# Performance work log

Measured on AMD Instinct MI355X. Metric: run time of the kernel, lower is better.

The kernel has to match this reference:

```python
import jax, jax.numpy as jnp
import numpy as np

B, S, D = 4, 2048, 1024

def setup_inputs() -> dict:
    key = jax.random.key(0)
    kv, kk, kq, kw = jax.random.split(key, 4)
    scale = 1.0 / np.sqrt(D)
    v = jax.random.normal(kv, (B, S, D), dtype=jnp.float32)
    k = jax.random.normal(kk, (B, S, D), dtype=jnp.float32)
    q = jax.random.normal(kq, (B, S, D), dtype=jnp.float32)
    wi = jax.random.normal(kw, (D, D), dtype=jnp.float32) * scale
    mask = jnp.tril(jnp.ones((S, S), dtype=bool))[None, :, :]  # causal [1,S,S]
    return {"v": v, "k": k, "q": q, "wi": wi, "mask": mask}

def reference(v, k, q, wi, mask):
    # project q, k, v with the shared weight wi
    q = q @ wi
    k = k @ wi
    v = v @ wi
    # scaled dot-product scores [B,S,S]
    scores = jnp.einsum('bqd,bkd->bqk', q, k) / jnp.sqrt(jnp.asarray(q.shape[-1], q.dtype))
    scores = jnp.where(mask, scores, jnp.asarray(-1e10, scores.dtype))
    attn = jax.nn.softmax(scores, axis=-1)
    # residual: q + attn @ v
    return q + jnp.einsum('bqk,bkd->bqd', attn, v)
```

## Files before the change

kernel.cpp:

```cpp
#include <hip/hip_runtime.h>
#include <hip/hip_bf16.h>

typedef __hip_bfloat16 bf16;
typedef short bf16x8 __attribute__((ext_vector_type(8)));
typedef float f32x4 __attribute__((ext_vector_type(4)));

#define HT 16384

__device__ __forceinline__ void gload16(const void* g, void* l) {
    __builtin_amdgcn_global_load_lds(
        (const __attribute__((address_space(1))) void*)g,
        (__attribute__((address_space(3))) void*)l, 16, 0, 0);
}

__device__ __forceinline__ void stage_half(char* lds, const bf16* src, int ld,
                                           int rowbase, int k0, int slotIdx,
                                           int tid)
{
    char* dst = lds + (size_t)slotIdx * HT + tid * 16;
    const int sub = tid >> 3;
    const int cb  = ((tid & 7) ^ (sub & 7)) << 4;
    #pragma unroll
    for (int p = 0; p < 2; ++p) {
        const int row = p * 64 + sub;
        const char* g = (const char*)(src + (size_t)(rowbase + row) * ld + k0) + cb;
        gload16(g, dst + p * 8192);
    }
}

__device__ __forceinline__ bf16x8 ldsfrag(const char* lds, int slotIdx,
                                          int row, int ks, int cb0)
{
    return *(const bf16x8*)(lds + (size_t)slotIdx * HT
                            + row * 128 + (cb0 ^ (ks << 6)));
}

__device__ __forceinline__ float bf2f(short s) {
    union { float f; unsigned u; } c;
    c.u = ((unsigned)(unsigned short)s) << 16;
    return c.f;
}

__launch_bounds__(512, 2)
__global__ void proj_bn128(const bf16* __restrict__ A, const bf16* __restrict__ B,
                           bf16* __restrict__ C)
{
    extern __shared__ char lds[];
    const int orig = blockIdx.y * 8 + blockIdx.x;
    const int wk = (orig & 7) * 96 + (orig >> 3);
    const int bi = wk >> 3, bj = wk & 7;
    const int brow = bi * 256, bcol = bj * 128;

    const int tid  = threadIdx.x;
    const int lane = tid & 63;
    const int w    = tid >> 6;
    const int wm   = w >> 1, wn = w & 1;
    const int fr   = lane & 15, fq = lane >> 4;
    const int cb0  = ((fr & 7) ^ fq) << 4;
    const int slotA = wm >> 1;
    const int rA    = (wm & 1) * 64;
    const int rB    = wn * 64;
    const int NT    = 16;

    f32x4 acc[4][4] = {};
    bf16x8 af[4][2], bv[4][2];

    stage_half(lds, B, 1024, bcol,       0, 2, tid);
    stage_half(lds, A, 1024, brow,       0, 0, tid);
    stage_half(lds, A, 1024, brow + 128, 0, 1, tid);
    stage_half(lds, B, 1024, bcol,      64, 5, tid);
    asm volatile("s_waitcnt vmcnt(2)" ::: "memory");
    __builtin_amdgcn_s_barrier();

#define QUAD2(m0, n0)                                                         \
    _Pragma("unroll") for (int dm = 0; dm < 2; ++dm)                          \
    _Pragma("unroll") for (int dn = 0; dn < 2; ++dn)                          \
    _Pragma("unroll") for (int ks = 0; ks < 2; ++ks)                          \
        acc[(m0)+dm][(n0)+dn] = __builtin_amdgcn_mfma_f32_16x16x32_bf16(      \
            af[(m0)+dm][ks], bv[(n0)+dn][ks], acc[(m0)+dm][(n0)+dn], 0, 0, 0);

    for (int t = 0; t < NT; ++t) {
        const int buf = t & 1, nbuf = buf ^ 1;
        const int k1 = min(t + 1, NT - 1) << 6;
        const int k2 = min(t + 2, NT - 1) << 6;

        #pragma unroll
        for (int m = 0; m < 2; ++m)
            #pragma unroll
            for (int ks = 0; ks < 2; ++ks)
                af[m][ks] = ldsfrag(lds, buf * 3 + slotA, rA + m * 16 + fr, ks, cb0);
        #pragma unroll
        for (int n = 0; n < 2; ++n)
            #pragma unroll
            for (int ks = 0; ks < 2; ++ks)
                bv[n][ks] = ldsfrag(lds, buf * 3 + 2, rB + n * 16 + fr, ks, cb0);
        stage_half(lds, A, 1024, brow, k1, nbuf * 3 + 0, tid);
        __builtin_amdgcn_s_barrier();
        __builtin_amdgcn_s_setprio(1);
        QUAD2(0, 0)
        __builtin_amdgcn_s_setprio(0);
        __builtin_amdgcn_s_barrier();

        #pragma unroll
        for (int n = 2; n < 4; ++n)
            #pragma unroll
            for (int ks = 0; ks < 2; ++ks)
                bv[n][ks] = ldsfrag(lds, buf * 3 + 2, rB + n * 16 + fr, ks, cb0);
        stage_half(lds, A, 1024, brow + 128, k1, nbuf * 3 + 1, tid);
        __builtin_amdgcn_s_barrier();
        __builtin_amdgcn_s_setprio(1);
        QUAD2(0, 2)
        __builtin_amdgcn_s_setprio(0);
        __builtin_amdgcn_s_barrier();

        #pragma unroll
        for (int m = 2; m < 4; ++m)
            #pragma unroll
            for (int ks = 0; ks < 2; ++ks)
                af[m][ks] = ldsfrag(lds, buf * 3 + slotA, rA + m * 16 + fr, ks, cb0);
        stage_half(lds, B, 1024, bcol, k2, buf * 3 + 2, tid);
        __builtin_amdgcn_s_barrier();
        __builtin_amdgcn_s_setprio(1);
        QUAD2(2, 2)
        __builtin_amdgcn_s_setprio(0);
        __builtin_amdgcn_s_barrier();

        __builtin_amdgcn_s_setprio(1);
        QUAD2(2, 0)
        __builtin_amdgcn_s_setprio(0);
        asm volatile("s_waitcnt vmcnt(2)" ::: "memory");
        __builtin_amdgcn_s_barrier();
    }
#undef QUAD2

    #pragma unroll
    for (int mf = 0; mf < 4; ++mf) {
        const int r0 = brow + wm * 64 + mf * 16 + fq * 4;
        #pragma unroll
        for (int nf = 0; nf < 4; ++nf) {
            const int c = bcol + wn * 64 + nf * 16 + fr;
            #pragma unroll
            for (int j = 0; j < 4; ++j)
                C[(size_t)(r0 + j) * 1024 + c] = __float2bfloat16(acc[mf][nf][j]);
        }
    }
}

template<int MODE>
__device__ __forceinline__ void tile128(char* lds, const bf16* A, const bf16* B,
                                        bf16* Cb, float* Cf, const bf16* Res,
                                        int lda, int ldb, int ldcb,
                                        int brow, int bcol, int NT, float scale,
                                        int tid, int wm, int wn, int fr, int fq,
                                        int cb0)
{
    f32x4 acc[4][2] = {};
    bf16x8 af[4][2], bv[2][2];

    stage_half(lds, A, lda, brow, 0,  0, tid);
    stage_half(lds, B, ldb, bcol, 0,  3, tid);
    stage_half(lds, A, lda, brow, 64, 1, tid);
    stage_half(lds, B, ldb, bcol, 64, 4, tid);
    asm volatile("s_waitcnt vmcnt(4)" ::: "memory");
    __builtin_amdgcn_s_barrier();

    for (int t = 0; t < NT; ++t) {
        const int aslot = t % 3, bslot = 3 + (t & 1);
        const int k2 = min(t + 2, NT - 1) << 6;

        #pragma unroll
        for (int m = 0; m < 2; ++m)
            #pragma unroll
            for (int ks = 0; ks < 2; ++ks)
                af[m][ks] = ldsfrag(lds, aslot, wm * 64 + m * 16 + fr, ks, cb0);
        #pragma unroll
        for (int n = 0; n < 2; ++n)
            #pragma unroll
            for (int ks = 0; ks < 2; ++ks)
                bv[n][ks] = ldsfrag(lds, bslot, wn * 32 + n * 16 + fr, ks, cb0);
        stage_half(lds, A, lda, brow, k2, (t + 2) % 3, tid);
        __builtin_amdgcn_s_barrier();
        __builtin_amdgcn_s_setprio(1);
        #pragma unroll
        for (int m = 0; m < 2; ++m)
            #pragma unroll
            for (int n = 0; n < 2; ++n)
                #pragma unroll
                for (int ks = 0; ks < 2; ++ks)
                    acc[m][n] = __builtin_amdgcn_mfma_f32_16x16x32_bf16(
                        af[m][ks], bv[n][ks], acc[m][n], 0, 0, 0);
        __builtin_amdgcn_s_setprio(0);
        __builtin_amdgcn_s_barrier();

        #pragma unroll
        for (int m = 2; m < 4; ++m)
            #pragma unroll
            for (int ks = 0; ks < 2; ++ks)
                af[m][ks] = ldsfrag(lds, aslot, wm * 64 + m * 16 + fr, ks, cb0);
        stage_half(lds, B, ldb, bcol, k2, bslot, tid);
        __builtin_amdgcn_s_barrier();
        __builtin_amdgcn_s_setprio(1);
        #pragma unroll
        for (int m = 2; m < 4; ++m)
            #pragma unroll
            for (int n = 0; n < 2; ++n)
                #pragma unroll
                for (int ks = 0; ks < 2; ++ks)
                    acc[m][n] = __builtin_amdgcn_mfma_f32_16x16x32_bf16(
                        af[m][ks], bv[n][ks], acc[m][n], 0, 0, 0);
        __builtin_amdgcn_s_setprio(0);
        asm volatile("s_waitcnt vmcnt(4)" ::: "memory");
        __builtin_amdgcn_s_barrier();
    }

    #pragma unroll
    for (int mf = 0; mf < 4; ++mf) {
        const int r0 = brow + wm * 64 + mf * 16 + fq * 4;
        #pragma unroll
        for (int nf = 0; nf < 2; ++nf) {
            const int c = bcol + wn * 32 + nf * 16 + fr;
            #pragma unroll
            for (int j = 0; j < 4; ++j) {
                if (MODE == 1)
                    Cb[(size_t)(r0 + j) * ldcb + c] =
                        __float2bfloat16(acc[mf][nf][j] * scale);
                else
                    Cf[(size_t)(r0 + j) * ldcb + c] = acc[mf][nf][j] +
                        __bfloat162float(Res[(size_t)(r0 + j) * ldcb + c]);
            }
        }
    }
}

__launch_bounds__(512, 4)
__global__ void scores128(const bf16* __restrict__ qp, const bf16* __restrict__ kp,
                          bf16* __restrict__ P)
{
    extern __shared__ char lds[];
    const int j = blockIdx.x;
    int bi = (int)((__fsqrt_rn(8.0f * j + 1.0f) - 1.0f) * 0.5f);
    while ((bi + 1) * (bi + 2) / 2 <= j) ++bi;
    while (bi * (bi + 1) / 2 > j) --bi;
    const int bj = j - bi * (bi + 1) / 2;
    const int bz = blockIdx.z;

    const int tid  = threadIdx.x;
    const int lane = tid & 63;
    const int w    = tid >> 6;
    const int wm   = w >> 2, wn = w & 3;
    const int fr   = lane & 15, fq = lane >> 4;
    const int cb0  = ((fr & 7) ^ fq) << 4;

    tile128<1>(lds,
               qp + (size_t)bz * 2048 * 1024,
               kp + (size_t)bz * 2048 * 1024,
               P + (size_t)bz * 2048 * 2048, nullptr, nullptr,
               1024, 1024, 2048,
               bi * 128, bj * 128, 16, 0.03125f,
               tid, wm, wn, fr, fq, cb0);
}

__launch_bounds__(512, 4)
__global__ void pv128(const bf16* __restrict__ P, const bf16* __restrict__ V,
                      const bf16* __restrict__ R, float* __restrict__ C)
{
    extern __shared__ char lds[];
    const int pid = blockIdx.x, bj = blockIdx.y, bz = blockIdx.z;
    const bf16* Pb = P + (size_t)bz * 2048 * 2048;
    const bf16* Vb = V + (size_t)bz * 1024 * 2048;
    const bf16* Rb = R + (size_t)bz * 2048 * 1024;
    float* Cb = C + (size_t)bz * 2048 * 1024;

    const int tid  = threadIdx.x;
    const int lane = tid & 63;
    const int w    = tid >> 6;
    const int wm   = w >> 2, wn = w & 3;
    const int fr   = lane & 15, fq = lane >> 4;
    const int cb0  = ((fr & 7) ^ fq) << 4;
    const int bcol = bj * 128;

    tile128<2>(lds, Pb, Vb, nullptr, Cb, Rb, 2048, 2048, 1024,
               pid * 128, bcol, 2 * (pid + 1), 1.0f,
               tid, wm, wn, fr, fq, cb0);
    asm volatile("s_waitcnt vmcnt(0) lgkmcnt(0)" ::: "memory");
    __builtin_amdgcn_s_barrier();
    const int bi2 = 15 - pid;
    tile128<2>(lds, Pb, Vb, nullptr, Cb, Rb, 2048, 2048, 1024,
               bi2 * 128, bcol, 2 * (bi2 + 1), 1.0f,
               tid, wm, wn, fr, fq, cb0);
}

__global__ void convert_qkv(const float* __restrict__ q, const float* __restrict__ k,
                            const float* __restrict__ v, bf16* __restrict__ Xb)
{
    const int N8 = 8192 * 1024 / 8;
    const int total = 3 * N8;
    for (int i = blockIdx.x * 256 + threadIdx.x; i < total; i += gridDim.x * 256) {
        const int t = i / N8, j = i - t * N8;
        const float4* s = (t == 0) ? (const float4*)q
                        : (t == 1) ? (const float4*)k : (const float4*)v;
        float4 a = s[2 * j], bq = s[2 * j + 1];
        float vals[8] = {a.x, a.y, a.z, a.w, bq.x, bq.y, bq.z, bq.w};
        union { short h[8]; bf16x8 v8; } o;
        #pragma unroll
        for (int e = 0; e < 8; ++e) {
            bf16 hh = __float2bfloat16(vals[e]);
            o.h[e] = *(short*)&hh;
        }
        ((bf16x8*)Xb)[i] = o.v8;
    }
}

__global__ void transpose_wi(const float* __restrict__ wi, bf16* __restrict__ Wt)
{
    __shared__ float t[32][33];
    const int n0 = blockIdx.x * 32, k0 = blockIdx.y * 32;
    const int lx = threadIdx.x & 31, ly = threadIdx.x >> 5;
    for (int i = ly; i < 32; i += 8)
        t[i][lx] = wi[(size_t)(k0 + i) * 1024 + n0 + lx];
    __syncthreads();
    for (int i = ly; i < 32; i += 8)
        Wt[(size_t)(n0 + i) * 1024 + k0 + lx] = __float2bfloat16(t[lx][i]);
}

__global__ void transpose_vp(const bf16* __restrict__ vp, bf16* __restrict__ vpT)
{
    __shared__ bf16 t[32][33];
    const int b = blockIdx.z;
    const int d0 = blockIdx.x * 32, s0 = blockIdx.y * 32;
    const bf16* src = vp + (size_t)b * 2048 * 1024;
    bf16* dst = vpT + (size_t)b * 1024 * 2048;
    const int lx = threadIdx.x & 31, ly = threadIdx.x >> 5;
    for (int i = ly; i < 32; i += 8)
        t[i][lx] = src[(size_t)(s0 + i) * 1024 + d0 + lx];
    __syncthreads();
    for (int i = ly; i < 32; i += 8)
        dst[(size_t)(d0 + i) * 2048 + s0 + lx] = t[lx][i];
}

__launch_bounds__(256)
__global__ void softmax_rows(bf16* __restrict__ P)
{
    const int wid = threadIdx.x >> 6, lane = threadIdx.x & 63;
    const int r = blockIdx.x * 4 + wid, b = blockIdx.y;
    bf16* row = P + ((size_t)b * 2048 + r) * 2048;
    const int nv  = r + 1;
    const int rup = (r & ~255) + 256;

    float vals[4][8];
    float m = -1e30f;
    #pragma unroll
    for (int c = 0; c < 4; ++c) {
        const int k0 = c * 512 + lane * 8;
        if (k0 < rup) {
            bf16x8 x = *(const bf16x8*)(row + k0);
            #pragma unroll
            for (int j = 0; j < 8; ++j) {
                float f = (k0 + j < nv) ? bf2f(x[j]) : -1e30f;
                vals[c][j] = f;
                m = fmaxf(m, f);
            }
        } else {
            #pragma unroll
            for (int j = 0; j < 8; ++j) vals[c][j] = -1e30f;
        }
    }
    #pragma unroll
    for (int o = 32; o; o >>= 1) m = fmaxf(m, __shfl_xor(m, o));

    float sum = 0.f;
    #pragma unroll
    for (int c = 0; c < 4; ++c)
        #pragma unroll
        for (int j = 0; j < 8; ++j) {
            float e = __expf(vals[c][j] - m);
            vals[c][j] = e;
            sum += e;
        }
    #pragma unroll
    for (int o = 32; o; o >>= 1) sum += __shfl_xor(sum, o);
    const float inv = 1.0f / sum;

    #pragma unroll
    for (int c = 0; c < 4; ++c) {
        const int k0 = c * 512 + lane * 8;
        if (k0 < rup) {
            union { short h[8]; bf16x8 v8; } o;
            #pragma unroll
            for (int j = 0; j < 8; ++j) {
                bf16 hh = __float2bfloat16(vals[c][j] * inv);
                o.h[j] = *(short*)&hh;
            }
            *(bf16x8*)(row + k0) = o.v8;
        }
    }
}

extern "C" void kernel_launch(void* const* d_in, const int* in_sizes, int n_in,
                              void* d_out, int out_size, void* d_ws, size_t ws_size,
                              hipStream_t stream)
{
    const float* v  = (const float*)d_in[0];
    const float* k  = (const float*)d_in[1];
    const float* q  = (const float*)d_in[2];
    const float* wi = (const float*)d_in[3];
    float* out = (float*)d_out;

    char* ws = (char*)d_ws;
    const size_t WT_OFF   = 0;
    const size_t PROJ_OFF = WT_OFF + (2u << 20);
    const size_t VPT_OFF  = PROJ_OFF + (size_t)24576 * 1024 * 2;
    const size_t XB_OFF   = VPT_OFF + (size_t)4 * 1024 * 2048 * 2;

    bf16* Wt   = (bf16*)(ws + WT_OFF);
    bf16* proj = (bf16*)(ws + PROJ_OFF);
    bf16* vpT  = (bf16*)(ws + VPT_OFF);
    bf16* Xb   = (bf16*)(ws + XB_OFF);
    bf16* P    = Xb;

    bf16* qp_b = proj;
    bf16* kp_b = proj + (size_t)8192 * 1024;
    bf16* vp_b = proj + (size_t)16384 * 1024;

    (void)hipFuncSetAttribute((const void*)proj_bn128,
            hipFuncAttributeMaxDynamicSharedMemorySize, 98304);
    (void)hipFuncSetAttribute((const void*)scores128,
            hipFuncAttributeMaxDynamicSharedMemorySize, 81920);
    (void)hipFuncSetAttribute((const void*)pv128,
            hipFuncAttributeMaxDynamicSharedMemorySize, 81920);

    transpose_wi<<<dim3(32, 32), 256, 0, stream>>>(wi, Wt);
    convert_qkv<<<2048, 256, 0, stream>>>(q, k, v, Xb);

    proj_bn128<<<dim3(8, 96), 512, 98304, stream>>>(Xb, Wt, proj);

    transpose_vp<<<dim3(32, 64, 4), 256, 0, stream>>>(vp_b, vpT);

    scores128<<<dim3(136, 1, 4), 512, 81920, stream>>>(qp_b, kp_b, P);

    softmax_rows<<<dim3(512, 4), 256, 0, stream>>>(P);

    pv128<<<dim3(8, 8, 4), 512, 81920, stream>>>(P, vpT, qp_b, out);
}
```

Measured before the change: 183.7 us.

## Fuse V transpose into projection epilogue and split-K warps in attention tiles

The projection kernel now writes the V projection directly in transposed layout from its epilogue, so the separate transpose_vp kernel and its extra global round trip go away. The shared tile128 routine is restructured so that pairs of waves split the K dimension, each computing a full 64x64 subtile, with the partial sums reduced through LDS before the epilogue. The pv128 grid is reordered so batch varies fastest within blockIdx.x, and softmax_rows now rounds its read bound to 128 columns instead of 256. The transposed V stores are strided short4 writes that may coalesce poorly, and the split-K reduction adds an LDS pass plus more accumulator registers per wave.

```diff
diff --git a/kernel.cpp b/kernel.cpp
--- a/kernel.cpp
+++ b/kernel.cpp
@@ -43,12 +43,12 @@
 
 __launch_bounds__(512, 2)
 __global__ void proj_bn128(const bf16* __restrict__ A, const bf16* __restrict__ B,
-                           bf16* __restrict__ C)
+                           bf16* __restrict__ C, bf16* __restrict__ vpT)
 {
     extern __shared__ char lds[];
     const int orig = blockIdx.y * 8 + blockIdx.x;
-    const int wk = (orig & 7) * 96 + (orig >> 3);
-    const int bi = wk >> 3, bj = wk & 7;
+    const int wk2 = (orig & 7) * 96 + (orig >> 3);
+    const int bi = wk2 >> 3, bj = wk2 & 7;
     const int brow = bi * 256, bcol = bj * 128;
 
     const int tid  = threadIdx.x;
@@ -133,15 +133,36 @@
     }
 #undef QUAD2
 
-    #pragma unroll
-    for (int mf = 0; mf < 4; ++mf) {
-        const int r0 = brow + wm * 64 + mf * 16 + fq * 4;
-        #pragma unroll
-        for (int nf = 0; nf < 4; ++nf) {
-            const int c = bcol + wn * 64 + nf * 16 + fr;
-            #pragma unroll
-            for (int j = 0; j < 4; ++j)
-                C[(size_t)(r0 + j) * 1024 + c] = __float2bfloat16(acc[mf][nf][j]);
+    if (brow < 16384) {
+        #pragma unroll
+        for (int mf = 0; mf < 4; ++mf) {
+            const int r0 = brow + wm * 64 + mf * 16 + fq * 4;
+            #pragma unroll
+            for (int nf = 0; nf < 4; ++nf) {
+                const int c = bcol + wn * 64 + nf * 16 + fr;
+                #pragma unroll
+                for (int j = 0; j < 4; ++j)
+                    C[(size_t)(r0 + j) * 1024 + c] = __float2bfloat16(acc[mf][nf][j]);
+            }
+        }
+    } else {
+        const int bb = (brow - 16384) >> 11;
+        bf16* vt = vpT + (size_t)bb * 1024 * 2048;
+        #pragma unroll
+        for (int mf = 0; mf < 4; ++mf) {
+            const int r0 = brow + wm * 64 + mf * 16 + fq * 4;
+            const int s0 = (r0 - 16384) & 2047;
+            #pragma unroll
+            for (int nf = 0; nf < 4; ++nf) {
+                const int c = bcol + wn * 64 + nf * 16 + fr;
+                union { short h[4]; short4 v4; } o;
+                #pragma unroll
+                for (int j = 0; j < 4; ++j) {
+                    bf16 hh = __float2bfloat16(acc[mf][nf][j]);
+                    o.h[j] = *(short*)&hh;
+                }
+                *(short4*)(vt + (size_t)c * 2048 + s0) = o.v4;
+            }
         }
     }
 }
@@ -151,11 +172,18 @@
                                         bf16* Cb, float* Cf, const bf16* Res,
                                         int lda, int ldb, int ldcb,
                                         int brow, int bcol, int NT, float scale,
-                                        int tid, int wm, int wn, int fr, int fq,
-                                        int cb0)
-{
-    f32x4 acc[4][2] = {};
-    bf16x8 af[4][2], bv[2][2];
+                                        int tid)
+{
+    const int lane = tid & 63;
+    const int w    = tid >> 6;
+    const int wkk  = w & 1;
+    const int wn   = (w >> 1) & 1;
+    const int wm   = w >> 2;
+    const int fr   = lane & 15, fq = lane >> 4;
+    const int cb0  = ((fr & 7) ^ fq) << 4;
+
+    f32x4 acc[4][4] = {};
+    bf16x8 af[4], bv[4];
 
     stage_half(lds, A, lda, brow, 0,  0, tid);
     stage_half(lds, B, ldb, bcol, 0,  3, tid);
@@ -169,64 +197,74 @@
         const int k2 = min(t + 2, NT - 1) << 6;
 
         #pragma unroll
-        for (int m = 0; m < 2; ++m)
-            #pragma unroll
-            for (int ks = 0; ks < 2; ++ks)
-                af[m][ks] = ldsfrag(lds, aslot, wm * 64 + m * 16 + fr, ks, cb0);
-        #pragma unroll
-        for (int n = 0; n < 2; ++n)
-            #pragma unroll
-            for (int ks = 0; ks < 2; ++ks)
-                bv[n][ks] = ldsfrag(lds, bslot, wn * 32 + n * 16 + fr, ks, cb0);
+        for (int m = 0; m < 4; ++m)
+            af[m] = ldsfrag(lds, aslot, wm * 64 + m * 16 + fr, wkk, cb0);
+        #pragma unroll
+        for (int n = 0; n < 4; ++n)
+            bv[n] = ldsfrag(lds, bslot, wn * 64 + n * 16 + fr, wkk, cb0);
         stage_half(lds, A, lda, brow, k2, (t + 2) % 3, tid);
         __builtin_amdgcn_s_barrier();
         __builtin_amdgcn_s_setprio(1);
         #pragma unroll
-        for (int m = 0; m < 2; ++m)
+        for (int m = 0; m < 4; ++m)
             #pragma unroll
             for (int n = 0; n < 2; ++n)
+                acc[m][n] = __builtin_amdgcn_mfma_f32_16x16x32_bf16(
+                    af[m], bv[n], acc[m][n], 0, 0, 0);
+        __builtin_amdgcn_s_setprio(0);
+        __builtin_amdgcn_s_barrier();
+
+        stage_half(lds, B, ldb, bcol, k2, bslot, tid);
+        __builtin_amdgcn_s_barrier();
+        __builtin_amdgcn_s_setprio(1);
+        #pragma unroll
+        for (int m = 0; m < 4; ++m)
+            #pragma unroll
+            for (int n = 2; n < 4; ++n)
+                acc[m][n] = __builtin_amdgcn_mfma_f32_16x16x32_bf16(
+                    af[m], bv[n], acc[m][n], 0, 0, 0);
+        __builtin_amdgcn_s_setprio(0);
+        asm volatile("s_waitcnt vmcnt(4)" ::: "memory");
+        __builtin_amdgcn_s_barrier();
+    }
+
+    asm volatile("s_waitcnt vmcnt(0)" ::: "memory");
+    __builtin_amdgcn_s_barrier();
+
+    char* mb = lds + (size_t)(wm * 2 + wn) * 16384 + lane * 16;
+    if (wkk == 1) {
+        #pragma unroll
+        for (int m = 0; m < 4; ++m)
+            #pragma unroll
+            for (int n = 0; n < 4; ++n)
+                *(f32x4*)(mb + (m * 4 + n) * 1024) = acc[m][n];
+    }
+    asm volatile("s_waitcnt lgkmcnt(0)" ::: "memory");
+    __builtin_amdgcn_s_barrier();
+
+    if (wkk == 0) {
+        #pragma unroll
+        for (int m = 0; m < 4; ++m)
+            #pragma unroll
+            for (int n = 0; n < 4; ++n) {
+                f32x4 o = *(const f32x4*)(mb + (m * 4 + n) * 1024);
+                acc[m][n] += o;
+            }
+        #pragma unroll
+        for (int mf = 0; mf < 4; ++mf) {
+            const int r0 = brow + wm * 64 + mf * 16 + fq * 4;
+            #pragma unroll
+            for (int nf = 0; nf < 4; ++nf) {
+                const int c = bcol + wn * 64 + nf * 16 + fr;
                 #pragma unroll
-                for (int ks = 0; ks < 2; ++ks)
-                    acc[m][n] = __builtin_amdgcn_mfma_f32_16x16x32_bf16(
-                        af[m][ks], bv[n][ks], acc[m][n], 0, 0, 0);
-        __builtin_amdgcn_s_setprio(0);
-        __builtin_amdgcn_s_barrier();
-
-        #pragma unroll
-        for (int m = 2; m < 4; ++m)
-            #pragma unroll
-            for (int ks = 0; ks < 2; ++ks)
-                af[m][ks] = ldsfrag(lds, aslot, wm * 64 + m * 16 + fr, ks, cb0);
-        stage_half(lds, B, ldb, bcol, k2, bslot, tid);
-        __builtin_amdgcn_s_barrier();
-        __builtin_amdgcn_s_setprio(1);
-        #pragma unroll
-        for (int m = 2; m < 4; ++m)
-            #pragma unroll
-            for (int n = 0; n < 2; ++n)
-                #pragma unroll
-                for (int ks = 0; ks < 2; ++ks)
-                    acc[m][n] = __builtin_amdgcn_mfma_f32_16x16x32_bf16(
-                        af[m][ks], bv[n][ks], acc[m][n], 0, 0, 0);
-        __builtin_amdgcn_s_setprio(0);
-        asm volatile("s_waitcnt vmcnt(4)" ::: "memory");
-        __builtin_amdgcn_s_barrier();
-    }
-
-    #pragma unroll
-    for (int mf = 0; mf < 4; ++mf) {
-        const int r0 = brow + wm * 64 + mf * 16 + fq * 4;
-        #pragma unroll
-        for (int nf = 0; nf < 2; ++nf) {
-            const int c = bcol + wn * 32 + nf * 16 + fr;
-            #pragma unroll
-            for (int j = 0; j < 4; ++j) {
-                if (MODE == 1)
-                    Cb[(size_t)(r0 + j) * ldcb + c] =
-                        __float2bfloat16(acc[mf][nf][j] * scale);
-                else
-                    Cf[(size_t)(r0 + j) * ldcb + c] = acc[mf][nf][j] +
-                        __bfloat162float(Res[(size_t)(r0 + j) * ldcb + c]);
+                for (int j = 0; j < 4; ++j) {
+                    if (MODE == 1)
+                        Cb[(size_t)(r0 + j) * ldcb + c] =
+                            __float2bfloat16(acc[mf][nf][j] * scale);
+                    else
+                        Cf[(size_t)(r0 + j) * ldcb + c] = acc[mf][nf][j] +
+                            __bfloat162float(Res[(size_t)(r0 + j) * ldcb + c]);
+                }
             }
         }
     }
@@ -244,20 +282,12 @@
     const int bj = j - bi * (bi + 1) / 2;
     const int bz = blockIdx.z;
 
-    const int tid  = threadIdx.x;
-    const int lane = tid & 63;
-    const int w    = tid >> 6;
-    const int wm   = w >> 2, wn = w & 3;
-    const int fr   = lane & 15, fq = lane >> 4;
-    const int cb0  = ((fr & 7) ^ fq) << 4;
-
     tile128<1>(lds,
                qp + (size_t)bz * 2048 * 1024,
                kp + (size_t)bz * 2048 * 1024,
                P + (size_t)bz * 2048 * 2048, nullptr, nullptr,
                1024, 1024, 2048,
-               bi * 128, bj * 128, 16, 0.03125f,
-               tid, wm, wn, fr, fq, cb0);
+               bi * 128, bj * 128, 16, 0.03125f, threadIdx.x);
 }
 
 __launch_bounds__(512, 4)
@@ -265,29 +295,23 @@
                       const bf16* __restrict__ R, float* __restrict__ C)
 {
     extern __shared__ char lds[];
-    const int pid = blockIdx.x, bj = blockIdx.y, bz = blockIdx.z;
+    const int g = blockIdx.x;
+    const int pid = g >> 2, bz = g & 3;
+    const int bj = blockIdx.y;
     const bf16* Pb = P + (size_t)bz * 2048 * 2048;
     const bf16* Vb = V + (size_t)bz * 1024 * 2048;
     const bf16* Rb = R + (size_t)bz * 2048 * 1024;
     float* Cb = C + (size_t)bz * 2048 * 1024;
-
-    const int tid  = threadIdx.x;
-    const int lane = tid & 63;
-    const int w    = tid >> 6;
-    const int wm   = w >> 2, wn = w & 3;
-    const int fr   = lane & 15, fq = lane >> 4;
-    const int cb0  = ((fr & 7) ^ fq) << 4;
     const int bcol = bj * 128;
+    const int tid = threadIdx.x;
 
     tile128<2>(lds, Pb, Vb, nullptr, Cb, Rb, 2048, 2048, 1024,
-               pid * 128, bcol, 2 * (pid + 1), 1.0f,
-               tid, wm, wn, fr, fq, cb0);
+               pid * 128, bcol, 2 * (pid + 1), 1.0f, tid);
     asm volatile("s_waitcnt vmcnt(0) lgkmcnt(0)" ::: "memory");
     __builtin_amdgcn_s_barrier();
     const int bi2 = 15 - pid;
     tile128<2>(lds, Pb, Vb, nullptr, Cb, Rb, 2048, 2048, 1024,
-               bi2 * 128, bcol, 2 * (bi2 + 1), 1.0f,
-               tid, wm, wn, fr, fq, cb0);
+               bi2 * 128, bcol, 2 * (bi2 + 1), 1.0f, tid);
 }
 
 __global__ void convert_qkv(const float* __restrict__ q, const float* __restrict__ k,
@@ -323,21 +347,6 @@
         Wt[(size_t)(n0 + i) * 1024 + k0 + lx] = __float2bfloat16(t[lx][i]);
 }
 
-__global__ void transpose_vp(const bf16* __restrict__ vp, bf16* __restrict__ vpT)
-{
-    __shared__ bf16 t[32][33];
-    const int b = blockIdx.z;
-    const int d0 = blockIdx.x * 32, s0 = blockIdx.y * 32;
-    const bf16* src = vp + (size_t)b * 2048 * 1024;
-    bf16* dst = vpT + (size_t)b * 1024 * 2048;
-    const int lx = threadIdx.x & 31, ly = threadIdx.x >> 5;
-    for (int i = ly; i < 32; i += 8)
-        t[i][lx] = src[(size_t)(s0 + i) * 1024 + d0 + lx];
-    __syncthreads();
-    for (int i = ly; i < 32; i += 8)
-        dst[(size_t)(d0 + i) * 2048 + s0 + lx] = t[lx][i];
-}
-
 __launch_bounds__(256)
 __global__ void softmax_rows(bf16* __restrict__ P)
 {
@@ -345,7 +354,7 @@
     const int r = blockIdx.x * 4 + wid, b = blockIdx.y;
     bf16* row = P + ((size_t)b * 2048 + r) * 2048;
     const int nv  = r + 1;
-    const int rup = (r & ~255) + 256;
+    const int rup = (r & ~127) + 128;
 
     float vals[4][8];
     float m = -1e30f;
@@ -420,7 +429,6 @@
 
     bf16* qp_b = proj;
     bf16* kp_b = proj + (size_t)8192 * 1024;
-    bf16* vp_b = proj + (size_t)16384 * 1024;
 
     (void)hipFuncSetAttribute((const void*)proj_bn128,
             hipFuncAttributeMaxDynamicSharedMemorySize, 98304);
@@ -432,13 +440,11 @@
     transpose_wi<<<dim3(32, 32), 256, 0, stream>>>(wi, Wt);
     convert_qkv<<<2048, 256, 0, stream>>>(q, k, v, Xb);
 
-    proj_bn128<<<dim3(8, 96), 512, 98304, stream>>>(Xb, Wt, proj);
-
-    transpose_vp<<<dim3(32, 64, 4), 256, 0, stream>>>(vp_b, vpT);
+    proj_bn128<<<dim3(8, 96), 512, 98304, stream>>>(Xb, Wt, proj, vpT);
 
     scores128<<<dim3(136, 1, 4), 512, 81920, stream>>>(qp_b, kp_b, P);
 
     softmax_rows<<<dim3(512, 4), 256, 0, stream>>>(P);
 
-    pv128<<<dim3(8, 8, 4), 512, 81920, stream>>>(P, vpT, qp_b, out);
-}
+    pv128<<<dim3(32, 8), 512, 81920, stream>>>(P, vpT, qp_b, out);
+}
```

After: 186.7 us. About the same (+1.6%).
